# Kernel tuning notes

Measured on AMD Instinct MI355X. Metric: run time of the kernel, lower is better.

Reference implementation:

```python
import jax, jax.numpy as jnp
import numpy as np

HEADS, HDIM, GROUPS, EPS = 8, 64, 8, 1e-5

def setup_inputs() -> dict:
    key = jax.random.key(0)
    ks = jax.random.split(key, 3)
    c, inner = 256, HEADS * HDIM
    return {
        "x": jax.random.normal(ks[0], (2, c, 16, 16, 16), dtype=jnp.float32),
        "gamma": jnp.ones((c,), jnp.float32),
        "beta": jnp.zeros((c,), jnp.float32),
        "w_qkv": jax.random.normal(ks[1], (3 * inner, c), dtype=jnp.float32) * (c ** -0.5),
        "b_qkv": jnp.zeros((3 * inner,), jnp.float32),
        "w_out": jax.random.normal(ks[2], (c, inner), dtype=jnp.float32) * (inner ** -0.5),
        "b_out": jnp.zeros((c,), jnp.float32),
    }

def reference(x, gamma, beta, w_qkv, b_qkv, w_out, b_out):
    b, c, d, h, w = x.shape
    n = d * h * w
    scale = HDIM ** -0.5
    # GroupNorm(8, c)
    xg = x.reshape(b, GROUPS, c // GROUPS, d, h, w)
    mu = xg.mean(axis=(2, 3, 4, 5), keepdims=True)
    var = xg.var(axis=(2, 3, 4, 5), keepdims=True)
    xn = ((xg - mu) * jax.lax.rsqrt(var + EPS)).reshape(b, c, d, h, w)
    xn = xn * gamma[None, :, None, None, None] + beta[None, :, None, None, None]
    # 1x1x1 conv -> qkv, channel order (three, heads, dim)
    qkv = jnp.einsum('oc,bcdhw->bodhw', w_qkv, xn) + b_qkv[None, :, None, None, None]
    qkv = qkv.reshape(b, 3, HEADS, HDIM, n).transpose(1, 0, 2, 4, 3)  # [3,b,heads,n,dim]
    q, k, v = qkv[0], qkv[1], qkv[2]
    attn = jax.nn.softmax(jnp.einsum('bhnd,bhmd->bhnm', q, k) * scale, axis=-1)
    out = jnp.einsum('bhnm,bhmd->bhnd', attn, v)  # [b,heads,n,dim]
    out = out.transpose(0, 1, 3, 2).reshape(b, HEADS * HDIM, d, h, w)  # (heads dim) channels
    y = jnp.einsum('oc,bcdhw->bodhw', w_out, out) + b_out[None, :, None, None, None]
    # Dropout(0.1) in eval mode = identity
    return y + x
```

## Files before the change

### kernel.cpp

```cpp
#include <hip/hip_runtime.h>
#include <hip/hip_bf16.h>


typedef __attribute__((ext_vector_type(8))) short bf8_t;
typedef __attribute__((ext_vector_type(4))) float f4_t;
typedef __attribute__((ext_vector_type(16))) float f16v;

#define NTOK 4096
#define GRP_ELEMS (32 * 4096)

__device__ __forceinline__ unsigned short f2bf(float f) {
  union { float f; unsigned int i; } v; v.f = f;
  unsigned int r = v.i + 0x7fffu + ((v.i >> 16) & 1u);
  return (unsigned short)(r >> 16);
}

__device__ __forceinline__ unsigned int pkbf(float a, float b) {
  float2 t; t.x = a; t.y = b;
  __hip_bfloat162 h = __float22bfloat162_rn(t);
  union { __hip_bfloat162 h; unsigned int u; } c; c.h = h;
  return c.u;
}

__device__ __forceinline__ void gl_lds16(const unsigned short* g, unsigned short* l) {
  __builtin_amdgcn_global_load_lds((const __attribute__((address_space(1))) void*)g,
                                   (__attribute__((address_space(3))) void*)l, 16, 0, 0);
}

__device__ __forceinline__ bf8_t ldsw128(const unsigned short* base, int row, int du) {
  return *(const bf8_t*)((const char*)base + (((row << 7) + (du << 4)) ^ ((row & 7) << 4)));
}
__device__ __forceinline__ bf8_t ldsw64(const unsigned short* base, int row, int du) {
  return *(const bf8_t*)((const char*)base + (((row << 6) + (du << 4)) ^ (((row >> 1) & 3) << 4)));
}

#if __has_builtin(__builtin_amdgcn_exp2f)
#define EXP2 __builtin_amdgcn_exp2f
#else
#define EXP2 exp2f
#endif

__global__ __launch_bounds__(256) void gn_stats_castw(const float* __restrict__ x, float* __restrict__ stats,
    const float* __restrict__ wqkv, const float* __restrict__ wout,
    unsigned short* __restrict__ wq, unsigned short* __restrict__ wo) {
  int bid = blockIdx.x;
  if (bid >= 256) {
    int i = (bid - 256) * 256 + threadIdx.x;
    const float* src; unsigned short* dst; int off;
    if (i < 98304) { src = wqkv; dst = wq; off = i; }
    else           { src = wout; dst = wo; off = i - 98304; }
    float4 v = ((const float4*)src)[off];
    union { unsigned short s[4]; uint2 u; } o;
    o.s[0] = f2bf(v.x); o.s[1] = f2bf(v.y); o.s[2] = f2bf(v.z); o.s[3] = f2bf(v.w);
    *(uint2*)(dst + (size_t)off * 4) = o.u;
    return;
  }
  int g = bid & 15, sp = bid >> 4;
  const float4* p = (const float4*)(x + (size_t)g * GRP_ELEMS + (size_t)sp * 8192);
  float s = 0.f, s2 = 0.f;
  for (int i = threadIdx.x; i < 2048; i += 256) {
    float4 v = p[i];
    s  += v.x + v.y + v.z + v.w;
    s2 += v.x * v.x + v.y * v.y + v.z * v.z + v.w * v.w;
  }
  for (int m = 32; m; m >>= 1) { s += __shfl_xor(s, m); s2 += __shfl_xor(s2, m); }
  __shared__ float rs[4][2];
  int wv = threadIdx.x >> 6;
  if ((threadIdx.x & 63) == 0) { rs[wv][0] = s; rs[wv][1] = s2; }
  __syncthreads();
  if (threadIdx.x == 0) {
    float ts = rs[0][0] + rs[1][0] + rs[2][0] + rs[3][0];
    float t2 = rs[0][1] + rs[1][1] + rs[2][1] + rs[3][1];
    atomicAdd(&stats[g], ts);
    atomicAdd(&stats[16 + g], t2);
  }
}

__global__ __launch_bounds__(256) void gn_apply(const float* __restrict__ x,
    const float* __restrict__ gamma, const float* __restrict__ beta,
    const float* __restrict__ stats, unsigned short* __restrict__ xnt) {
  __shared__ float t[64][65];
  int b = blockIdx.z, c0 = blockIdx.y * 64, n0 = blockIdx.x * 64;
  int tr = threadIdx.x >> 2;
  int tc = (threadIdx.x & 3) * 16;
  int c = c0 + tr;
  int g = b * 8 + (c >> 5);
  float mu = stats[g] * (1.f / GRP_ELEMS);
  float var = stats[16 + g] * (1.f / GRP_ELEMS) - mu * mu;
  float rstd = rsqrtf(var + 1e-5f);
  float sc = gamma[c] * rstd;
  float sh = beta[c] - mu * sc;
  const float* xp = x + ((size_t)(b * 256 + c)) * NTOK + n0 + tc;
  for (int q = 0; q < 4; ++q) {
    float4 v = *(const float4*)(xp + q * 4);
    t[tr][tc + q * 4 + 0] = v.x * sc + sh;
    t[tr][tc + q * 4 + 1] = v.y * sc + sh;
    t[tr][tc + q * 4 + 2] = v.z * sc + sh;
    t[tr][tc + q * 4 + 3] = v.w * sc + sh;
  }
  __syncthreads();
  int n = n0 + tr;
  union { unsigned short s[16]; uint4 u[2]; } tmp;
  for (int q = 0; q < 16; ++q) tmp.s[q] = f2bf(t[tc + q][tr]);
  uint4* dst = (uint4*)(xnt + ((size_t)b * NTOK + n) * 256 + c0 + tc);
  dst[0] = tmp.u[0];
  dst[1] = tmp.u[1];
}

__global__ __launch_bounds__(256) void qkv_gemm(const unsigned short* __restrict__ wq,
    const unsigned short* __restrict__ xnt, const float* __restrict__ bqkv,
    unsigned short* __restrict__ Qg, unsigned short* __restrict__ Kg, unsigned short* __restrict__ Vt) {
  __shared__ unsigned short Al[2][4096];
  __shared__ unsigned short Bl[2][4096];
  int b = blockIdx.z, m0 = blockIdx.y * 128, n0 = blockIdx.x * 128;
  const unsigned short* Ap = wq + (size_t)m0 * 256;
  const unsigned short* Bp = xnt + ((size_t)b * NTOK + n0) * 256;
  int lane = threadIdx.x & 63, wv = threadIdx.x >> 6;
  int lq = lane & 15, hq = lane >> 4;
  int m_off = (wv >> 1) * 64, n_off = (wv & 1) * 64;
  f4_t acc[4][4] = {};
  {
    for (int is = 0; is < 2; ++is) {
      int ck = wv * 128 + is * 64 + lane;
      int r = ck >> 2, cu = ck & 3;
      int csw = (cu ^ ((r >> 1) & 3)) << 3;
      gl_lds16(Ap + (size_t)r * 256 + csw, &Al[0][(wv * 128 + is * 64) * 8]);
      gl_lds16(Bp + (size_t)r * 256 + csw, &Bl[0][(wv * 128 + is * 64) * 8]);
    }
  }
  __syncthreads();
  for (int kt = 0; kt < 8; ++kt) {
    int cb = kt & 1, nb = cb ^ 1;
    if (kt < 7) {
      int k0 = (kt + 1) * 32;
      for (int is = 0; is < 2; ++is) {
        int ck = wv * 128 + is * 64 + lane;
        int r = ck >> 2, cu = ck & 3;
        int csw = (cu ^ ((r >> 1) & 3)) << 3;
        gl_lds16(Ap + (size_t)r * 256 + k0 + csw, &Al[nb][(wv * 128 + is * 64) * 8]);
        gl_lds16(Bp + (size_t)r * 256 + k0 + csw, &Bl[nb][(wv * 128 + is * 64) * 8]);
      }
    }
    const unsigned short* Ac = Al[cb];
    const unsigned short* Bc = Bl[cb];
    bf8_t af[4], bfr[4];
    for (int i = 0; i < 4; ++i) af[i]  = ldsw64(Ac, m_off + i * 16 + lq, hq);
    for (int j = 0; j < 4; ++j) bfr[j] = ldsw64(Bc, n_off + j * 16 + lq, hq);
    for (int i = 0; i < 4; ++i)
      for (int j = 0; j < 4; ++j)
        acc[i][j] = __builtin_amdgcn_mfma_f32_16x16x32_bf16(af[i], bfr[j], acc[i][j], 0, 0, 0);
    __syncthreads();
  }
  int tq = m0 >> 9;
  if (tq < 2) {
    unsigned short* dst = tq == 0 ? Qg : Kg;
    float sc = tq == 0 ? 0.1803368801111243f : 1.0f;
    for (int i = 0; i < 4; ++i)
      for (int j = 0; j < 4; ++j) {
        int o0 = m0 + m_off + i * 16 + hq * 4;
        int n = n0 + n_off + j * 16 + lq;
        int h = (o0 >> 6) & 7, dd0 = o0 & 63;
        size_t bh = (size_t)b * 8 + h;
        uint2 pk;
        pk.x = pkbf((acc[i][j][0] + bqkv[o0 + 0]) * sc, (acc[i][j][1] + bqkv[o0 + 1]) * sc);
        pk.y = pkbf((acc[i][j][2] + bqkv[o0 + 2]) * sc, (acc[i][j][3] + bqkv[o0 + 3]) * sc);
        *(uint2*)(dst + (bh * NTOK + n) * 64 + dd0) = pk;
      }
  } else {
    for (int i = 0; i < 4; ++i)
      for (int j = 0; j < 4; ++j) {
        int n = n0 + n_off + j * 16 + lq;
        for (int jj = 0; jj < 4; ++jj) {
          int o = m0 + m_off + i * 16 + hq * 4 + jj;
          int h = (o >> 6) & 7, dd = o & 63;
          size_t bh = (size_t)b * 8 + h;
          Vt[(bh * 64 + dd) * NTOK + n] = f2bf(acc[i][j][jj] + bqkv[o]);
        }
      }
  }
}

__global__ __launch_bounds__(128) void attn(const unsigned short* __restrict__ Qg,
    const unsigned short* __restrict__ Kg, const unsigned short* __restrict__ Vt,
    unsigned short* __restrict__ att) {
  __shared__ unsigned short Kls[2][4096];
  __shared__ unsigned short Vls[2][4096];
  int bid = blockIdx.x;
  int bh = (bid & 7) * 2 + (bid >> 9);
  int q0 = ((bid >> 3) & 63) * 64;
  int b = bh >> 3, h = bh & 7;
  const unsigned short* kp = Kg + (size_t)bh * NTOK * 64;
  const unsigned short* vp = Vt + (size_t)bh * 64 * NTOK;
  int tid = threadIdx.x;
  int lane = tid & 63, wv = tid >> 6;
  int l31 = lane & 31, h5 = lane >> 5;
  const unsigned short* qp = Qg + ((size_t)bh * NTOK + q0 + wv * 32 + l31) * 64;
  bf8_t aq[4];
  for (int t4 = 0; t4 < 4; ++t4)
    aq[t4] = *(const bf8_t*)(qp + t4 * 16 + h5 * 8);
  f16v accO[2] = {};
  float ls = 0.f;
  {
    for (int is = 0; is < 4; ++is) {
      int ck = is * 128 + tid;
      int r = ck >> 3, cu = ck & 7;
      int csw = (cu ^ (r & 7)) << 3;
      gl_lds16(kp + (size_t)r * 64 + csw, &Kls[0][ck * 8]);
      gl_lds16(vp + (size_t)r * NTOK + csw, &Vls[0][ck * 8]);
    }
  }
  __syncthreads();
  #pragma unroll 2
  for (int t = 0; t < 64; ++t) {
    int cb = t & 1, nb = cb ^ 1;
    if (t < 63) {
      int tn = t + 1;
      for (int is = 0; is < 4; ++is) {
        int ck = is * 128 + tid;
        int r = ck >> 3, cu = ck & 7;
        int csw = (cu ^ (r & 7)) << 3;
        gl_lds16(kp + (size_t)(tn * 64 + r) * 64 + csw, &Kls[nb][ck * 8]);
        gl_lds16(vp + (size_t)r * NTOK + tn * 64 + csw, &Vls[nb][ck * 8]);
      }
    }
    const unsigned short* Kc = Kls[cb];
    const unsigned short* Vc = Vls[cb];
    f16v s[2] = {};
    __builtin_amdgcn_s_setprio(1);
    #pragma unroll
    for (int t4 = 0; t4 < 4; ++t4) {
      bf8_t ak0 = ldsw128(Kc, l31, 2 * t4 + h5);
      bf8_t ak1 = ldsw128(Kc, 32 + l31, 2 * t4 + h5);
      s[0] = __builtin_amdgcn_mfma_f32_32x32x16_bf16(ak0, aq[t4], s[0], 0, 0, 0);
      s[1] = __builtin_amdgcn_mfma_f32_32x32x16_bf16(ak1, aq[t4], s[1], 0, 0, 0);
    }
    __builtin_amdgcn_s_setprio(0);
    float rs = 0.f;
    #pragma unroll
    for (int kvb = 0; kvb < 2; ++kvb)
      #pragma unroll
      for (int r = 0; r < 16; ++r) {
        float p = EXP2(s[kvb][r]);
        s[kvb][r] = p;
        rs += p;
      }
    ls += rs;
    bf8_t pb[4];
    #pragma unroll
    for (int t4 = 0; t4 < 4; ++t4) {
      int kvb = t4 >> 1, r0 = (t4 & 1) * 8;
      unsigned int pA0 = pkbf(s[kvb][r0 + 0], s[kvb][r0 + 1]);
      unsigned int pA1 = pkbf(s[kvb][r0 + 2], s[kvb][r0 + 3]);
      unsigned int pB0 = pkbf(s[kvb][r0 + 4], s[kvb][r0 + 5]);
      unsigned int pB1 = pkbf(s[kvb][r0 + 6], s[kvb][r0 + 7]);
      unsigned int send0 = h5 ? pA0 : pB0;
      unsigned int send1 = h5 ? pA1 : pB1;
      unsigned int recv0 = __shfl_xor(send0, 32);
      unsigned int recv1 = __shfl_xor(send1, 32);
      union { unsigned int u[4]; bf8_t v; } pk;
      pk.u[0] = h5 ? recv0 : pA0;
      pk.u[1] = h5 ? recv1 : pA1;
      pk.u[2] = h5 ? pB0 : recv0;
      pk.u[3] = h5 ? pB1 : recv1;
      pb[t4] = pk.v;
    }
    __builtin_amdgcn_s_setprio(1);
    #pragma unroll
    for (int t4 = 0; t4 < 4; ++t4) {
      bf8_t av0 = ldsw128(Vc, l31, 2 * t4 + h5);
      bf8_t av1 = ldsw128(Vc, 32 + l31, 2 * t4 + h5);
      accO[0] = __builtin_amdgcn_mfma_f32_32x32x16_bf16(av0, pb[t4], accO[0], 0, 0, 0);
      accO[1] = __builtin_amdgcn_mfma_f32_32x32x16_bf16(av1, pb[t4], accO[1], 0, 0, 0);
    }
    __builtin_amdgcn_s_setprio(0);
    __syncthreads();
  }
  ls += __shfl_xor(ls, 32);
  float inv = 1.0f / ls;
  int q = q0 + wv * 32 + l31;
  unsigned short* op = att + ((size_t)b * NTOK + q) * 512 + h * 64;
  #pragma unroll
  for (int db = 0; db < 2; ++db)
    #pragma unroll
    for (int g = 0; g < 4; ++g) {
      uint2 pk;
      pk.x = pkbf(accO[db][g * 4 + 0] * inv, accO[db][g * 4 + 1] * inv);
      pk.y = pkbf(accO[db][g * 4 + 2] * inv, accO[db][g * 4 + 3] * inv);
      *(uint2*)(op + db * 32 + g * 8 + h5 * 4) = pk;
    }
}

__global__ __launch_bounds__(256) void out_proj(const unsigned short* __restrict__ wo,
    const unsigned short* __restrict__ att, const float* __restrict__ bout,
    const float* __restrict__ x, float* __restrict__ y) {
  __shared__ unsigned short Al[2][2048];
  __shared__ unsigned short Bl[2][4096];
  int b = blockIdx.z, m0 = blockIdx.y * 64, n0 = blockIdx.x * 128;
  const unsigned short* Ap = wo + (size_t)m0 * 512;
  const unsigned short* Bp = att + ((size_t)b * NTOK + n0) * 512;
  int lane = threadIdx.x & 63, wv = threadIdx.x >> 6;
  int lq = lane & 15, hq = lane >> 4;
  int m_off = (wv >> 1) * 32, n_off = (wv & 1) * 64;
  f4_t acc[2][4] = {};
  {
    int ckA = wv * 64 + lane;
    int rA = ckA >> 2, cuA = ckA & 3;
    gl_lds16(Ap + (size_t)rA * 512 + ((cuA ^ ((rA >> 1) & 3)) << 3), &Al[0][(wv * 64) * 8]);
    for (int is = 0; is < 2; ++is) {
      int ck = wv * 128 + is * 64 + lane;
      int r = ck >> 2, cu = ck & 3;
      gl_lds16(Bp + (size_t)r * 512 + ((cu ^ ((r >> 1) & 3)) << 3), &Bl[0][(wv * 128 + is * 64) * 8]);
    }
  }
  __syncthreads();
  for (int kt = 0; kt < 16; ++kt) {
    int cb = kt & 1, nb = cb ^ 1;
    if (kt < 15) {
      int k0 = (kt + 1) * 32;
      int ckA = wv * 64 + lane;
      int rA = ckA >> 2, cuA = ckA & 3;
      gl_lds16(Ap + (size_t)rA * 512 + k0 + ((cuA ^ ((rA >> 1) & 3)) << 3), &Al[nb][(wv * 64) * 8]);
      for (int is = 0; is < 2; ++is) {
        int ck = wv * 128 + is * 64 + lane;
        int r = ck >> 2, cu = ck & 3;
        gl_lds16(Bp + (size_t)r * 512 + k0 + ((cu ^ ((r >> 1) & 3)) << 3), &Bl[nb][(wv * 128 + is * 64) * 8]);
      }
    }
    const unsigned short* Ac = Al[cb];
    const unsigned short* Bc = Bl[cb];
    bf8_t af[2], bfr[4];
    for (int i = 0; i < 2; ++i) af[i]  = ldsw64(Ac, m_off + i * 16 + lq, hq);
    for (int j = 0; j < 4; ++j) bfr[j] = ldsw64(Bc, n_off + j * 16 + lq, hq);
    for (int i = 0; i < 2; ++i)
      for (int j = 0; j < 4; ++j)
        acc[i][j] = __builtin_amdgcn_mfma_f32_16x16x32_bf16(af[i], bfr[j], acc[i][j], 0, 0, 0);
    __syncthreads();
  }
  for (int i = 0; i < 2; ++i)
    for (int j = 0; j < 4; ++j) {
      int n = n0 + n_off + j * 16 + lq;
      for (int jj = 0; jj < 4; ++jj) {
        int co = m0 + m_off + i * 16 + hq * 4 + jj;
        size_t idx = ((size_t)b * 256 + co) * NTOK + n;
        y[idx] = acc[i][j][jj] + bout[co] + x[idx];
      }
    }
}

extern "C" void kernel_launch(void* const* d_in, const int* in_sizes, int n_in,
                              void* d_out, int out_size, void* d_ws, size_t ws_size,
                              hipStream_t stream) {
  const float* x     = (const float*)d_in[0];
  const float* gamma = (const float*)d_in[1];
  const float* beta  = (const float*)d_in[2];
  const float* wqkv  = (const float*)d_in[3];
  const float* bqkv  = (const float*)d_in[4];
  const float* wout  = (const float*)d_in[5];
  const float* bout  = (const float*)d_in[6];
  float* y = (float*)d_out;

  char* ws = (char*)d_ws;
  float*          stats = (float*)ws;
  unsigned short* WQ    = (unsigned short*)(ws + 256);
  unsigned short* WO    = (unsigned short*)(ws + 786688);
  unsigned short* XNT   = (unsigned short*)(ws + 1048832);
  unsigned short* Qg    = (unsigned short*)(ws + 5243136);
  unsigned short* Kg    = (unsigned short*)(ws + 13631744);
  unsigned short* Vt    = (unsigned short*)(ws + 22020352);
  unsigned short* ATT   = (unsigned short*)(ws + 30408960);

  hipMemsetAsync(stats, 0, 128, stream);
  gn_stats_castw<<<768, 256, 0, stream>>>(x, stats, wqkv, wout, WQ, WO);
  gn_apply<<<dim3(64, 4, 2), 256, 0, stream>>>(x, gamma, beta, stats, XNT);
  qkv_gemm<<<dim3(32, 12, 2), 256, 0, stream>>>(WQ, XNT, bqkv, Qg, Kg, Vt);
  attn<<<1024, 128, 0, stream>>>(Qg, Kg, Vt, ATT);
  out_proj<<<dim3(32, 4, 2), 256, 0, stream>>>(WO, ATT, bout, x, y);
}
```

Baseline: 219.7 us.

## Split attention KV range across two blocks with atomic bf16 accumulation

Result: slower. 299.9 us (+36.5%).

```diff
diff --git a/kernel.cpp b/kernel.cpp
--- a/kernel.cpp
+++ b/kernel.cpp
@@ -22,6 +22,11 @@
   return c.u;
 }
 
+__device__ __forceinline__ __hip_bfloat162 bf2(float a, float b) {
+  float2 t; t.x = a; t.y = b;
+  return __float22bfloat162_rn(t);
+}
+
 __device__ __forceinline__ void gl_lds16(const unsigned short* g, unsigned short* l) {
   __builtin_amdgcn_global_load_lds((const __attribute__((address_space(1))) void*)g,
                                    (__attribute__((address_space(3))) void*)l, 16, 0, 0);
@@ -39,6 +44,11 @@
 #else
 #define EXP2 exp2f
 #endif
+
+#define LGKM0() do { asm volatile("s_waitcnt lgkmcnt(0)" ::: "memory"); \
+                     __builtin_amdgcn_sched_barrier(0); } while (0)
+#define WAITVM8() asm volatile("s_waitcnt vmcnt(8)" ::: "memory")
+#define WAITVM0() asm volatile("s_waitcnt vmcnt(0)" ::: "memory")
 
 __global__ __launch_bounds__(256) void gn_stats_castw(const float* __restrict__ x, float* __restrict__ stats,
     const float* __restrict__ wqkv, const float* __restrict__ wout,
@@ -180,169 +190,206 @@
   }
 }
 
-__global__ __launch_bounds__(128) void attn(const unsigned short* __restrict__ Qg,
+__global__ __launch_bounds__(64, 2) void attn(const unsigned short* __restrict__ Qg,
     const unsigned short* __restrict__ Kg, const unsigned short* __restrict__ Vt,
-    unsigned short* __restrict__ att) {
-  __shared__ unsigned short Kls[2][4096];
-  __shared__ unsigned short Vls[2][4096];
+    __hip_bfloat162* __restrict__ att, float* __restrict__ lsum) {
+  __shared__ unsigned short Kls[2][2048];
+  __shared__ unsigned short Vls[2][2048];
   int bid = blockIdx.x;
-  int bh = (bid & 7) * 2 + (bid >> 9);
-  int q0 = ((bid >> 3) & 63) * 64;
+  int qt = bid >> 5, j = (bid >> 3) & 3, xcd = bid & 7;
+  int combo = xcd * 4 + j;
+  int half = combo >> 4, bh = combo & 15;
+  int q0 = qt * 64;
   int b = bh >> 3, h = bh & 7;
+  int kvbase = half * 2048;
   const unsigned short* kp = Kg + (size_t)bh * NTOK * 64;
   const unsigned short* vp = Vt + (size_t)bh * 64 * NTOK;
-  int tid = threadIdx.x;
-  int lane = tid & 63, wv = tid >> 6;
+  int lane = threadIdx.x;
   int l31 = lane & 31, h5 = lane >> 5;
-  const unsigned short* qp = Qg + ((size_t)bh * NTOK + q0 + wv * 32 + l31) * 64;
-  bf8_t aq[4];
-  for (int t4 = 0; t4 < 4; ++t4)
-    aq[t4] = *(const bf8_t*)(qp + t4 * 16 + h5 * 8);
-  f16v accO[2] = {};
-  float ls = 0.f;
-  {
-    for (int is = 0; is < 4; ++is) {
-      int ck = is * 128 + tid;
-      int r = ck >> 3, cu = ck & 7;
-      int csw = (cu ^ (r & 7)) << 3;
-      gl_lds16(kp + (size_t)r * 64 + csw, &Kls[0][ck * 8]);
-      gl_lds16(vp + (size_t)r * NTOK + csw, &Vls[0][ck * 8]);
-    }
-  }
-  __syncthreads();
-  #pragma unroll 2
-  for (int t = 0; t < 64; ++t) {
-    int cb = t & 1, nb = cb ^ 1;
-    if (t < 63) {
-      int tn = t + 1;
-      for (int is = 0; is < 4; ++is) {
-        int ck = is * 128 + tid;
-        int r = ck >> 3, cu = ck & 7;
-        int csw = (cu ^ (r & 7)) << 3;
-        gl_lds16(kp + (size_t)(tn * 64 + r) * 64 + csw, &Kls[nb][ck * 8]);
-        gl_lds16(vp + (size_t)r * NTOK + tn * 64 + csw, &Vls[nb][ck * 8]);
-      }
-    }
-    const unsigned short* Kc = Kls[cb];
-    const unsigned short* Vc = Vls[cb];
-    f16v s[2] = {};
-    __builtin_amdgcn_s_setprio(1);
+
+  bf8_t aq[2][4];
+  const unsigned short* qp = Qg + ((size_t)bh * NTOK + q0) * 64;
+  #pragma unroll
+  for (int qb = 0; qb < 2; ++qb)
     #pragma unroll
-    for (int t4 = 0; t4 < 4; ++t4) {
-      bf8_t ak0 = ldsw128(Kc, l31, 2 * t4 + h5);
-      bf8_t ak1 = ldsw128(Kc, 32 + l31, 2 * t4 + h5);
-      s[0] = __builtin_amdgcn_mfma_f32_32x32x16_bf16(ak0, aq[t4], s[0], 0, 0, 0);
-      s[1] = __builtin_amdgcn_mfma_f32_32x32x16_bf16(ak1, aq[t4], s[1], 0, 0, 0);
-    }
-    __builtin_amdgcn_s_setprio(0);
-    float rs = 0.f;
-    #pragma unroll
-    for (int kvb = 0; kvb < 2; ++kvb)
-      #pragma unroll
-      for (int r = 0; r < 16; ++r) {
-        float p = EXP2(s[kvb][r]);
-        s[kvb][r] = p;
-        rs += p;
-      }
-    ls += rs;
-    bf8_t pb[4];
-    #pragma unroll
-    for (int t4 = 0; t4 < 4; ++t4) {
-      int kvb = t4 >> 1, r0 = (t4 & 1) * 8;
-      unsigned int pA0 = pkbf(s[kvb][r0 + 0], s[kvb][r0 + 1]);
-      unsigned int pA1 = pkbf(s[kvb][r0 + 2], s[kvb][r0 + 3]);
-      unsigned int pB0 = pkbf(s[kvb][r0 + 4], s[kvb][r0 + 5]);
-      unsigned int pB1 = pkbf(s[kvb][r0 + 6], s[kvb][r0 + 7]);
-      unsigned int send0 = h5 ? pA0 : pB0;
-      unsigned int send1 = h5 ? pA1 : pB1;
-      unsigned int recv0 = __shfl_xor(send0, 32);
-      unsigned int recv1 = __shfl_xor(send1, 32);
-      union { unsigned int u[4]; bf8_t v; } pk;
-      pk.u[0] = h5 ? recv0 : pA0;
-      pk.u[1] = h5 ? recv1 : pA1;
-      pk.u[2] = h5 ? pB0 : recv0;
-      pk.u[3] = h5 ? pB1 : recv1;
-      pb[t4] = pk.v;
-    }
-    __builtin_amdgcn_s_setprio(1);
-    #pragma unroll
-    for (int t4 = 0; t4 < 4; ++t4) {
-      bf8_t av0 = ldsw128(Vc, l31, 2 * t4 + h5);
-      bf8_t av1 = ldsw128(Vc, 32 + l31, 2 * t4 + h5);
-      accO[0] = __builtin_amdgcn_mfma_f32_32x32x16_bf16(av0, pb[t4], accO[0], 0, 0, 0);
-      accO[1] = __builtin_amdgcn_mfma_f32_32x32x16_bf16(av1, pb[t4], accO[1], 0, 0, 0);
-    }
-    __builtin_amdgcn_s_setprio(0);
-    __syncthreads();
-  }
-  ls += __shfl_xor(ls, 32);
-  float inv = 1.0f / ls;
-  int q = q0 + wv * 32 + l31;
-  unsigned short* op = att + ((size_t)b * NTOK + q) * 512 + h * 64;
+    for (int sl = 0; sl < 4; ++sl)
+      aq[qb][sl] = *(const bf8_t*)(qp + (size_t)(qb * 32 + l31) * 64 + sl * 16 + h5 * 8);
+
+  const unsigned short* ksrc[4];
+  const unsigned short* vsrc[4];
+  #pragma unroll
+  for (int i = 0; i < 4; ++i) {
+    int c = i * 64 + lane;
+    int kr = c >> 3, kc = (c & 7) ^ (kr & 7);
+    ksrc[i] = kp + (size_t)(kvbase + kr) * 64 + kc * 8;
+    int vr = c >> 2, vc = (c & 3) ^ ((vr >> 1) & 3);
+    vsrc[i] = vp + (size_t)vr * NTOK + kvbase + vc * 8;
+  }
+
+#define STAGE(BUF) do { \
+    _Pragma("unroll") \
+    for (int i = 0; i < 4; ++i) { \
+      gl_lds16(ksrc[i], &Kls[BUF][(i * 64 + lane) * 8]); \
+      gl_lds16(vsrc[i], &Vls[BUF][(i * 64 + lane) * 8]); \
+    } \
+    _Pragma("unroll") \
+    for (int i = 0; i < 4; ++i) { ksrc[i] += 32 * 64; vsrc[i] += 32; } \
+  } while (0)
+
+  f16v accO[2][2] = {};
+  float ls0 = 0.f, ls1 = 0.f;
+
+  STAGE(0);
+  STAGE(1);
+
+#define BODY(CUR, DOSTAGE, LAST) do { \
+    if (LAST) { WAITVM0(); } else { WAITVM8(); } \
+    const unsigned short* Kc = Kls[CUR]; \
+    const unsigned short* Vc = Vls[CUR]; \
+    f16v sq0 = {}, sq1 = {}; \
+    __builtin_amdgcn_s_setprio(1); \
+    _Pragma("unroll") \
+    for (int sl = 0; sl < 4; ++sl) { \
+      bf8_t ak = ldsw128(Kc, l31, sl * 2 + h5); \
+      sq0 = __builtin_amdgcn_mfma_f32_32x32x16_bf16(ak, aq[0][sl], sq0, 0, 0, 0); \
+      sq1 = __builtin_amdgcn_mfma_f32_32x32x16_bf16(ak, aq[1][sl], sq1, 0, 0, 0); \
+    } \
+    __builtin_amdgcn_s_setprio(0); \
+    float r0 = 0.f, r1 = 0.f; \
+    _Pragma("unroll") \
+    for (int r = 0; r < 16; ++r) { \
+      float p0 = EXP2(sq0[r]); sq0[r] = p0; r0 += p0; \
+      float p1 = EXP2(sq1[r]); sq1[r] = p1; r1 += p1; \
+    } \
+    ls0 += r0; ls1 += r1; \
+    __builtin_amdgcn_s_setprio(1); \
+    _Pragma("unroll") \
+    for (int tp = 0; tp < 2; ++tp) { \
+      unsigned int g0a0 = pkbf(sq0[8 * tp + 0], sq0[8 * tp + 1]); \
+      unsigned int g0b0 = pkbf(sq0[8 * tp + 2], sq0[8 * tp + 3]); \
+      unsigned int g1a0 = pkbf(sq0[8 * tp + 4], sq0[8 * tp + 5]); \
+      unsigned int g1b0 = pkbf(sq0[8 * tp + 6], sq0[8 * tp + 7]); \
+      unsigned int g0a1 = pkbf(sq1[8 * tp + 0], sq1[8 * tp + 1]); \
+      unsigned int g0b1 = pkbf(sq1[8 * tp + 2], sq1[8 * tp + 3]); \
+      unsigned int g1a1 = pkbf(sq1[8 * tp + 4], sq1[8 * tp + 5]); \
+      unsigned int g1b1 = pkbf(sq1[8 * tp + 6], sq1[8 * tp + 7]); \
+      unsigned int ra0 = __shfl_xor(h5 ? g0a0 : g1a0, 32); \
+      unsigned int rb0 = __shfl_xor(h5 ? g0b0 : g1b0, 32); \
+      unsigned int ra1 = __shfl_xor(h5 ? g0a1 : g1a1, 32); \
+      unsigned int rb1 = __shfl_xor(h5 ? g0b1 : g1b1, 32); \
+      union { unsigned int u[4]; bf8_t v; } p0, p1; \
+      p0.u[0] = h5 ? ra0 : g0a0;  p0.u[1] = h5 ? rb0 : g0b0; \
+      p0.u[2] = h5 ? g1a0 : ra0;  p0.u[3] = h5 ? g1b0 : rb0; \
+      p1.u[0] = h5 ? ra1 : g0a1;  p1.u[1] = h5 ? rb1 : g0b1; \
+      p1.u[2] = h5 ? g1a1 : ra1;  p1.u[3] = h5 ? g1b1 : rb1; \
+      bf8_t av0 = ldsw64(Vc, l31, tp * 2 + h5); \
+      bf8_t av1 = ldsw64(Vc, 32 + l31, tp * 2 + h5); \
+      accO[0][0] = __builtin_amdgcn_mfma_f32_32x32x16_bf16(av0, p0.v, accO[0][0], 0, 0, 0); \
+      accO[0][1] = __builtin_amdgcn_mfma_f32_32x32x16_bf16(av0, p1.v, accO[0][1], 0, 0, 0); \
+      accO[1][0] = __builtin_amdgcn_mfma_f32_32x32x16_bf16(av1, p0.v, accO[1][0], 0, 0, 0); \
+      accO[1][1] = __builtin_amdgcn_mfma_f32_32x32x16_bf16(av1, p1.v, accO[1][1], 0, 0, 0); \
+    } \
+    __builtin_amdgcn_s_setprio(0); \
+    if (DOSTAGE) { LGKM0(); STAGE(CUR); } \
+  } while (0)
+
+  for (int tt = 0; tt < 31; ++tt) {
+    BODY(0, 1, 0);
+    BODY(1, 1, 0);
+  }
+  BODY(0, 0, 0);
+  BODY(1, 0, 1);
+
+  ls0 += __shfl_xor(ls0, 32);
+  ls1 += __shfl_xor(ls1, 32);
+  if (h5 == 0) {
+    atomicAdd(&lsum[(size_t)bh * NTOK + q0 + l31], ls0);
+    atomicAdd(&lsum[(size_t)bh * NTOK + q0 + 32 + l31], ls1);
+  }
   #pragma unroll
   for (int db = 0; db < 2; ++db)
     #pragma unroll
-    for (int g = 0; g < 4; ++g) {
-      uint2 pk;
-      pk.x = pkbf(accO[db][g * 4 + 0] * inv, accO[db][g * 4 + 1] * inv);
-      pk.y = pkbf(accO[db][g * 4 + 2] * inv, accO[db][g * 4 + 3] * inv);
-      *(uint2*)(op + db * 32 + g * 8 + h5 * 4) = pk;
+    for (int qb = 0; qb < 2; ++qb) {
+      int q = q0 + qb * 32 + l31;
+      __hip_bfloat162* base = att + (size_t)(b * NTOK + q) * 256 + (h * 64 + db * 32 + 4 * h5) / 2;
+      #pragma unroll
+      for (int g = 0; g < 4; ++g) {
+        unsafeAtomicAdd(base + 4 * g + 0, bf2(accO[db][qb][4 * g + 0], accO[db][qb][4 * g + 1]));
+        unsafeAtomicAdd(base + 4 * g + 1, bf2(accO[db][qb][4 * g + 2], accO[db][qb][4 * g + 3]));
+      }
     }
+#undef BODY
+#undef STAGE
+}
+
+__global__ __launch_bounds__(256) void attn_norm(unsigned short* __restrict__ att,
+                                                 const float* __restrict__ lsum) {
+  int gid = blockIdx.x * 256 + threadIdx.x;
+  int row = gid >> 5;
+  int ci0 = (gid & 31) * 16;
+  int b = row >> 12, n = row & 4095;
+  int h = ci0 >> 6;
+  float inv = 1.0f / lsum[(size_t)(b * 8 + h) * NTOK + n];
+  unsigned short* p = att + (size_t)row * 512 + ci0;
+  union { uint4 q; unsigned int u[4]; } v0, v1;
+  v0.q = *(uint4*)p; v1.q = *(uint4*)(p + 8);
+  #pragma unroll
+  for (int w = 0; w < 4; ++w) {
+    float lo = __uint_as_float(v0.u[w] << 16) * inv;
+    float hi = __uint_as_float(v0.u[w] & 0xffff0000u) * inv;
+    v0.u[w] = pkbf(lo, hi);
+    float lo1 = __uint_as_float(v1.u[w] << 16) * inv;
+    float hi1 = __uint_as_float(v1.u[w] & 0xffff0000u) * inv;
+    v1.u[w] = pkbf(lo1, hi1);
+  }
+  *(uint4*)p = v0.q;
+  *(uint4*)(p + 8) = v1.q;
 }
 
 __global__ __launch_bounds__(256) void out_proj(const unsigned short* __restrict__ wo,
     const unsigned short* __restrict__ att, const float* __restrict__ bout,
     const float* __restrict__ x, float* __restrict__ y) {
   __shared__ unsigned short Al[2][2048];
-  __shared__ unsigned short Bl[2][4096];
-  int b = blockIdx.z, m0 = blockIdx.y * 64, n0 = blockIdx.x * 128;
+  __shared__ unsigned short Bl[2][2048];
+  int b = blockIdx.z, m0 = blockIdx.y * 64, n0 = blockIdx.x * 64;
   const unsigned short* Ap = wo + (size_t)m0 * 512;
   const unsigned short* Bp = att + ((size_t)b * NTOK + n0) * 512;
   int lane = threadIdx.x & 63, wv = threadIdx.x >> 6;
   int lq = lane & 15, hq = lane >> 4;
-  int m_off = (wv >> 1) * 32, n_off = (wv & 1) * 64;
-  f4_t acc[2][4] = {};
+  int m_off = (wv >> 1) * 32, n_off = (wv & 1) * 32;
+  int ck = threadIdx.x;
+  int rr = ck >> 2, cu = ck & 3;
+  int csw = (cu ^ ((rr >> 1) & 3)) << 3;
+  f4_t acc[2][2] = {};
   {
-    int ckA = wv * 64 + lane;
-    int rA = ckA >> 2, cuA = ckA & 3;
-    gl_lds16(Ap + (size_t)rA * 512 + ((cuA ^ ((rA >> 1) & 3)) << 3), &Al[0][(wv * 64) * 8]);
-    for (int is = 0; is < 2; ++is) {
-      int ck = wv * 128 + is * 64 + lane;
-      int r = ck >> 2, cu = ck & 3;
-      gl_lds16(Bp + (size_t)r * 512 + ((cu ^ ((r >> 1) & 3)) << 3), &Bl[0][(wv * 128 + is * 64) * 8]);
-    }
+    gl_lds16(Ap + (size_t)rr * 512 + csw, &Al[0][ck * 8]);
+    gl_lds16(Bp + (size_t)rr * 512 + csw, &Bl[0][ck * 8]);
   }
   __syncthreads();
   for (int kt = 0; kt < 16; ++kt) {
     int cb = kt & 1, nb = cb ^ 1;
     if (kt < 15) {
       int k0 = (kt + 1) * 32;
-      int ckA = wv * 64 + lane;
-      int rA = ckA >> 2, cuA = ckA & 3;
-      gl_lds16(Ap + (size_t)rA * 512 + k0 + ((cuA ^ ((rA >> 1) & 3)) << 3), &Al[nb][(wv * 64) * 8]);
-      for (int is = 0; is < 2; ++is) {
-        int ck = wv * 128 + is * 64 + lane;
-        int r = ck >> 2, cu = ck & 3;
-        gl_lds16(Bp + (size_t)r * 512 + k0 + ((cu ^ ((r >> 1) & 3)) << 3), &Bl[nb][(wv * 128 + is * 64) * 8]);
-      }
+      gl_lds16(Ap + (size_t)rr * 512 + k0 + csw, &Al[nb][ck * 8]);
+      gl_lds16(Bp + (size_t)rr * 512 + k0 + csw, &Bl[nb][ck * 8]);
     }
     const unsigned short* Ac = Al[cb];
     const unsigned short* Bc = Bl[cb];
-    bf8_t af[2], bfr[4];
+    bf8_t af[2], bfr[2];
     for (int i = 0; i < 2; ++i) af[i]  = ldsw64(Ac, m_off + i * 16 + lq, hq);
-    for (int j = 0; j < 4; ++j) bfr[j] = ldsw64(Bc, n_off + j * 16 + lq, hq);
+    for (int jj = 0; jj < 2; ++jj) bfr[jj] = ldsw64(Bc, n_off + jj * 16 + lq, hq);
     for (int i = 0; i < 2; ++i)
-      for (int j = 0; j < 4; ++j)
-        acc[i][j] = __builtin_amdgcn_mfma_f32_16x16x32_bf16(af[i], bfr[j], acc[i][j], 0, 0, 0);
+      for (int jj = 0; jj < 2; ++jj)
+        acc[i][jj] = __builtin_amdgcn_mfma_f32_16x16x32_bf16(af[i], bfr[jj], acc[i][jj], 0, 0, 0);
     __syncthreads();
   }
   for (int i = 0; i < 2; ++i)
-    for (int j = 0; j < 4; ++j) {
-      int n = n0 + n_off + j * 16 + lq;
-      for (int jj = 0; jj < 4; ++jj) {
-        int co = m0 + m_off + i * 16 + hq * 4 + jj;
+    for (int jj = 0; jj < 2; ++jj) {
+      int n = n0 + n_off + jj * 16 + lq;
+      for (int e = 0; e < 4; ++e) {
+        int co = m0 + m_off + i * 16 + hq * 4 + e;
         size_t idx = ((size_t)b * 256 + co) * NTOK + n;
-        y[idx] = acc[i][j][jj] + bout[co] + x[idx];
+        y[idx] = acc[i][jj][e] + bout[co] + x[idx];
       }
     }
 }
@@ -364,6 +411,7 @@
   unsigned short* WQ    = (unsigned short*)(ws + 256);
   unsigned short* WO    = (unsigned short*)(ws + 786688);
   unsigned short* XNT   = (unsigned short*)(ws + 1048832);
+  float*          L     = (float*)(ws + 1048832);
   unsigned short* Qg    = (unsigned short*)(ws + 5243136);
   unsigned short* Kg    = (unsigned short*)(ws + 13631744);
   unsigned short* Vt    = (unsigned short*)(ws + 22020352);
@@ -373,6 +421,9 @@
   gn_stats_castw<<<768, 256, 0, stream>>>(x, stats, wqkv, wout, WQ, WO);
   gn_apply<<<dim3(64, 4, 2), 256, 0, stream>>>(x, gamma, beta, stats, XNT);
   qkv_gemm<<<dim3(32, 12, 2), 256, 0, stream>>>(WQ, XNT, bqkv, Qg, Kg, Vt);
-  attn<<<1024, 128, 0, stream>>>(Qg, Kg, Vt, ATT);
-  out_proj<<<dim3(32, 4, 2), 256, 0, stream>>>(WO, ATT, bout, x, y);
-}
+  hipMemsetAsync(ATT, 0, 8388608, stream);
+  hipMemsetAsync(L, 0, 262144, stream);
+  attn<<<2048, 64, 0, stream>>>(Qg, Kg, Vt, (__hip_bfloat162*)ATT, L);
+  attn_norm<<<1024, 256, 0, stream>>>(ATT, L);
+  out_proj<<<dim3(64, 4, 2), 256, 0, stream>>>(WO, ATT, bout, x, y);
+}
```
